# Kernel tuning notes

Measured on AMD Instinct MI355X. Metric: run time of the kernel, lower is better.

Reference implementation:

```python
import jax, jax.numpy as jnp
import numpy as np

NUM_EMBEDDINGS = 1024
EMBEDDING_DIM = 64
COMMIT_COST = 0.25


def setup_inputs() -> dict:
    key = jax.random.key(0)
    k1, k2 = jax.random.split(key)
    latent = jax.random.normal(k1, (32, EMBEDDING_DIM, 32, 32), dtype=jnp.float32)
    embedding_weight = jax.random.normal(k2, (NUM_EMBEDDINGS, EMBEDDING_DIM), dtype=jnp.float32)
    return {"latent": latent, "embedding_weight": embedding_weight}


def reference(latent, embedding_weight):
    # rearrange 'b n j d -> b j d n'; n == embedding_dim
    lat = jnp.transpose(latent, (0, 2, 3, 1))  # [b, j, d, n]
    flat = lat.reshape(-1, EMBEDDING_DIM)      # [T, D]
    # squared-euclidean distances [T, K]
    distances = (
        jnp.sum(flat ** 2, axis=1, keepdims=True)
        + jnp.sum(embedding_weight ** 2, axis=1)
        - 2.0 * flat @ embedding_weight.T
    )
    idx = jnp.argmin(distances, axis=1)                         # [T]
    encodings = jax.nn.one_hot(idx, NUM_EMBEDDINGS, dtype=flat.dtype)  # [T, K]
    quantized_flat = embedding_weight[idx]                      # gather == encodings @ W
    quantized = quantized_flat.reshape(lat.shape)               # [b, j, d, n]

    e_latent_loss = jnp.mean((jax.lax.stop_gradient(quantized) - lat) ** 2)
    loss = COMMIT_COST * e_latent_loss

    # straight-through estimator
    quantized_st = lat + jax.lax.stop_gradient(quantized - lat)

    avg_probs = jnp.mean(encodings, axis=0)
    perplexity = jnp.exp(-jnp.sum(avg_probs * jnp.log(avg_probs + 1e-10)))

    # rearrange back 'b j d n -> b n j d'
    quantized_out = jnp.transpose(quantized_st, (0, 3, 1, 2))
    return quantized_out, loss, perplexity, encodings, distances
```

## Files before the change

### kernel.cpp

```cpp
#include <hip/hip_runtime.h>
#include <cfloat>

#define T_TOTAL 32768
#define DIM 64
#define KCODES 1024

static constexpr long long OFF_Q    = 0;
static constexpr long long OFF_LOSS = 2097152;
static constexpr long long OFF_PERP = 2097153;
static constexpr long long OFF_ENC  = 2097154;
static constexpr long long OFF_DIST = 2097154LL + 33554432LL;


__global__ __launch_bounds__(256) void vq_prep_kernel(const float* __restrict__ W,
                                                      float* __restrict__ ww,
                                                      float* __restrict__ WT) {
    const int tid = threadIdx.x;
    if (blockIdx.x < 256) {
        const int lane = tid & 63;
        const int code = blockIdx.x * 4 + (tid >> 6);
        float v = W[code * DIM + lane];
        float s = v * v;
        #pragma unroll
        for (int off = 32; off > 0; off >>= 1)
            s += __shfl_down(s, off, 64);
        if (lane == 0) ww[code] = s;
    } else {
        const int n = blockIdx.x - 256;
        #pragma unroll
        for (int i = 0; i < 4; ++i) {
            int k = i * 256 + tid;
            WT[n * KCODES + k] = W[k * DIM + n];
        }
    }
}

__global__ __launch_bounds__(256, 4) void vq_main_kernel(const float* __restrict__ lat,
                                                         const float* __restrict__ W,
                                                         const float* __restrict__ ww,
                                                         const float* __restrict__ WT,
                                                         float* __restrict__ out,
                                                         int* __restrict__ counts,
                                                         float* __restrict__ lossSum) {
    __shared__ float xT[64 * 32];
    __shared__ float wS[8 * 512];
    __shared__ float xx[32];
    __shared__ int   selIdx[32];

    const int tid = threadIdx.x;
    const int ct  = tid & 63;
    const int rg  = tid >> 6;
    const int t0  = blockIdx.x * 32;
    const long long base = (long long)(t0 >> 10) * 65536 + (long long)(t0 & 1023);

    #pragma unroll
    for (int i = 0; i < 8; ++i) {
        int e  = i * 256 + tid;
        int n  = e >> 5;
        int tl = e & 31;
        xT[e] = lat[base + (long long)n * 1024 + tl];
    }
    __syncthreads();
    if (tid < 32) {
        float s = 0.f;
        #pragma unroll 8
        for (int n = 0; n < 64; ++n) {
            float v = xT[n * 32 + tid];
            s = fmaf(v, v, s);
        }
        xx[tid] = s;
    }

    float minV[8];
    int   minI[8];
    #pragma unroll
    for (int r = 0; r < 8; ++r) { minV[r] = FLT_MAX; minI[r] = 0; }

    float* __restrict__ distOut = out + OFF_DIST;

    for (int c = 0; c < 2; ++c) {
        float acc[8][8];
        #pragma unroll
        for (int r = 0; r < 8; ++r)
            #pragma unroll
            for (int k = 0; k < 8; ++k) acc[r][k] = 0.f;

        for (int sub = 0; sub < 8; ++sub) {
            __syncthreads();
            #pragma unroll
            for (int i = 0; i < 4; ++i) {
                int e  = i * 256 + tid;
                int n  = e >> 7;
                int k4 = (e & 127) * 4;
                *(float4*)&wS[n * 512 + k4] =
                    *(const float4*)&WT[(sub * 8 + n) * KCODES + c * 512 + k4];
            }
            __syncthreads();

            #pragma unroll
            for (int nn = 0; nn < 8; ++nn) {
                const int ng = sub * 8 + nn;
                float4 a0 = *(const float4*)&xT[ng * 32 + rg * 8];
                float4 a1 = *(const float4*)&xT[ng * 32 + rg * 8 + 4];
                float2 b0 = *(const float2*)&wS[nn * 512 + ct * 2];
                float2 b1 = *(const float2*)&wS[nn * 512 + ct * 2 + 128];
                float2 b2 = *(const float2*)&wS[nn * 512 + ct * 2 + 256];
                float2 b3 = *(const float2*)&wS[nn * 512 + ct * 2 + 384];
                float ar[8] = {a0.x, a0.y, a0.z, a0.w, a1.x, a1.y, a1.z, a1.w};
                float br[8] = {b0.x, b0.y, b1.x, b1.y, b2.x, b2.y, b3.x, b3.y};
                #pragma unroll
                for (int r = 0; r < 8; ++r)
                    #pragma unroll
                    for (int k = 0; k < 8; ++k)
                        acc[r][k] = fmaf(ar[r], br[k], acc[r][k]);
            }
        }

        const int kb = c * 512 + ct * 2;
        float2 wwv[4];
        #pragma unroll
        for (int j = 0; j < 4; ++j)
            wwv[j] = *(const float2*)&ww[kb + j * 128];
        #pragma unroll
        for (int r = 0; r < 8; ++r) {
            const int row = rg * 8 + r;
            const float xxr = xx[row];
            const long long ro = (long long)(t0 + row) * KCODES + kb;
            #pragma unroll
            for (int j = 0; j < 4; ++j) {
                float d0 = (xxr + wwv[j].x) - 2.f * acc[r][2 * j];
                float d1 = (xxr + wwv[j].y) - 2.f * acc[r][2 * j + 1];
                const int ki = kb + j * 128;
                if (d0 < minV[r]) { minV[r] = d0; minI[r] = ki; }
                if (d1 < minV[r]) { minV[r] = d1; minI[r] = ki + 1; }
                *(float2*)&distOut[ro + j * 128] = make_float2(d0, d1);
            }
        }
    }

    #pragma unroll
    for (int r = 0; r < 8; ++r) {
        float v  = minV[r];
        int   i0 = minI[r];
        #pragma unroll
        for (int off = 32; off > 0; off >>= 1) {
            float v2 = __shfl_down(v, off, 64);
            int   i2 = __shfl_down(i0, off, 64);
            if (v2 < v || (v2 == v && i2 < i0)) { v = v2; i0 = i2; }
        }
        if (ct == 0) {
            selIdx[rg * 8 + r] = i0;
            atomicAdd(&counts[i0], 1);
        }
    }
    __syncthreads();

    float* qS = wS;
    #pragma unroll
    for (int i = 0; i < 8; ++i) {
        int e   = i * 256 + tid;
        int row = e >> 6;
        int n   = e & 63;
        qS[row * 65 + n] = W[selIdx[row] * DIM + n];
    }
    __syncthreads();

    float ls = 0.f;
    #pragma unroll
    for (int i = 0; i < 2; ++i) {
        int e2  = i * 256 + tid;
        int n   = e2 >> 3;
        int tl0 = (e2 & 7) * 4;
        float q0 = qS[(tl0 + 0) * 65 + n];
        float q1 = qS[(tl0 + 1) * 65 + n];
        float q2 = qS[(tl0 + 2) * 65 + n];
        float q3 = qS[(tl0 + 3) * 65 + n];
        float x0 = xT[n * 32 + tl0 + 0];
        float x1 = xT[n * 32 + tl0 + 1];
        float x2 = xT[n * 32 + tl0 + 2];
        float x3 = xT[n * 32 + tl0 + 3];
        *(float4*)&out[OFF_Q + base + (long long)n * 1024 + tl0] = make_float4(q0, q1, q2, q3);
        float e0 = q0 - x0; ls = fmaf(e0, e0, ls);
        float e1 = q1 - x1; ls = fmaf(e1, e1, ls);
        float e2d = q2 - x2; ls = fmaf(e2d, e2d, ls);
        float e3 = q3 - x3; ls = fmaf(e3, e3, ls);
    }
    #pragma unroll
    for (int off = 32; off > 0; off >>= 1)
        ls += __shfl_down(ls, off, 64);
    if (ct == 0) atomicAdd(lossSum, ls);

    float* __restrict__ enc = out + OFF_ENC;
    #pragma unroll 4
    for (int i = 0; i < 64; ++i) {
        int e2  = i * 256 + tid;
        int row = e2 >> 9;
        int k2  = (e2 & 511) * 2;
        int sel = selIdx[row];
        float2 v;
        v.x = (k2     == sel) ? 1.f : 0.f;
        v.y = (k2 + 1 == sel) ? 1.f : 0.f;
        *(float2*)&enc[(long long)(t0 + row) * KCODES + k2] = v;
    }
}

__global__ __launch_bounds__(1024) void vq_finalize_kernel(const int* __restrict__ counts,
                                                           const float* __restrict__ lossSum,
                                                           float* __restrict__ out) {
    __shared__ float red[16];
    const int tid = threadIdx.x;
    float p = (float)counts[tid] * (1.0f / 32768.0f);
    float term = p * logf(p + 1e-10f);
    #pragma unroll
    for (int off = 32; off > 0; off >>= 1)
        term += __shfl_down(term, off, 64);
    if ((tid & 63) == 0) red[tid >> 6] = term;
    __syncthreads();
    if (tid == 0) {
        float s = 0.f;
        #pragma unroll
        for (int i = 0; i < 16; ++i) s += red[i];
        out[OFF_PERP] = expf(-s);
        out[OFF_LOSS] = 0.25f * lossSum[0] * (1.0f / 2097152.0f);
    }
}

extern "C" void kernel_launch(void* const* d_in, const int* in_sizes, int n_in,
                              void* d_out, int out_size, void* d_ws, size_t ws_size,
                              hipStream_t stream) {
    (void)in_sizes; (void)n_in; (void)out_size; (void)ws_size;
    const float* lat = (const float*)d_in[0];
    const float* W   = (const float*)d_in[1];
    float* out = (float*)d_out;

    int*   counts  = (int*)d_ws;
    float* ww      = (float*)((char*)d_ws + 4096);
    float* lossSum = (float*)((char*)d_ws + 8192);
    float* WT      = (float*)((char*)d_ws + 12288);

    hipMemsetAsync(d_ws, 0, 8192 + 16, stream);

    vq_prep_kernel<<<320, 256, 0, stream>>>(W, ww, WT);
    vq_main_kernel<<<1024, 256, 0, stream>>>(lat, W, ww, WT, out, counts, lossSum);
    vq_finalize_kernel<<<1, 1024, 0, stream>>>(counts, lossSum, out);
}
```

Before: 398.9 us.

## Read codebook directly from global, nontemporal stores, register-based one-hot writes

The main kernel drops the shared-memory staging of the transposed codebook and its per-subtile barriers. It now reads W^T straight from global/L2 in four 256-code chunks with a smaller 8x4 accumulator tile. The distance and one-hot encoding outputs use nontemporal stores, and each wave writes its own rows using the selected index broadcast in registers. The latent norm is fused into the load through shared atomics. The aim is to cut barriers and register pressure and to stream the large outputs past the cache, at the cost of more global loads per FMA.

```diff
diff --git a/kernel.cpp b/kernel.cpp
--- a/kernel.cpp
+++ b/kernel.cpp
@@ -4,6 +4,8 @@
 #define T_TOTAL 32768
 #define DIM 64
 #define KCODES 1024
+
+typedef float f32x2 __attribute__((ext_vector_type(2)));
 
 static constexpr long long OFF_Q    = 0;
 static constexpr long long OFF_LOSS = 2097152;
@@ -43,9 +45,9 @@
                                                          int* __restrict__ counts,
                                                          float* __restrict__ lossSum) {
     __shared__ float xT[64 * 32];
-    __shared__ float wS[8 * 512];
     __shared__ float xx[32];
-    __shared__ int   selIdx[32];
+    __shared__ float qS[32 * 65];
+    __shared__ int   selS[32];
 
     const int tid = threadIdx.x;
     const int ct  = tid & 63;
@@ -53,23 +55,22 @@
     const int t0  = blockIdx.x * 32;
     const long long base = (long long)(t0 >> 10) * 65536 + (long long)(t0 & 1023);
 
-    #pragma unroll
-    for (int i = 0; i < 8; ++i) {
-        int e  = i * 256 + tid;
-        int n  = e >> 5;
-        int tl = e & 31;
-        xT[e] = lat[base + (long long)n * 1024 + tl];
-    }
-    __syncthreads();
-    if (tid < 32) {
-        float s = 0.f;
-        #pragma unroll 8
-        for (int n = 0; n < 64; ++n) {
-            float v = xT[n * 32 + tid];
-            s = fmaf(v, v, s);
-        }
-        xx[tid] = s;
-    }
+    if (tid < 32) xx[tid] = 0.f;
+    __syncthreads();
+    {
+        float sp = 0.f;
+        #pragma unroll
+        for (int i = 0; i < 8; ++i) {
+            int e  = i * 256 + tid;
+            int n  = e >> 5;
+            int tl = e & 31;
+            float v = lat[base + (long long)n * 1024 + tl];
+            xT[e] = v;
+            sp = fmaf(v, v, sp);
+        }
+        atomicAdd(&xx[tid & 31], sp);
+    }
+    __syncthreads();
 
     float minV[8];
     int   minI[8];
@@ -78,66 +79,53 @@
 
     float* __restrict__ distOut = out + OFF_DIST;
 
-    for (int c = 0; c < 2; ++c) {
-        float acc[8][8];
+    for (int c = 0; c < 4; ++c) {
+        float acc[8][4];
         #pragma unroll
         for (int r = 0; r < 8; ++r)
             #pragma unroll
-            for (int k = 0; k < 8; ++k) acc[r][k] = 0.f;
-
-        for (int sub = 0; sub < 8; ++sub) {
-            __syncthreads();
+            for (int k = 0; k < 4; ++k) acc[r][k] = 0.f;
+
+        const float* __restrict__ wp = WT + c * 256 + ct * 2;
+        #pragma unroll 4
+        for (int n = 0; n < 64; ++n) {
+            float4 a0 = *(const float4*)&xT[n * 32 + rg * 8];
+            float4 a1 = *(const float4*)&xT[n * 32 + rg * 8 + 4];
+            float2 b0 = *(const float2*)&wp[n * KCODES];
+            float2 b1 = *(const float2*)&wp[n * KCODES + 128];
+            float ar[8] = {a0.x, a0.y, a0.z, a0.w, a1.x, a1.y, a1.z, a1.w};
+            float br[4] = {b0.x, b0.y, b1.x, b1.y};
             #pragma unroll
-            for (int i = 0; i < 4; ++i) {
-                int e  = i * 256 + tid;
-                int n  = e >> 7;
-                int k4 = (e & 127) * 4;
-                *(float4*)&wS[n * 512 + k4] =
-                    *(const float4*)&WT[(sub * 8 + n) * KCODES + c * 512 + k4];
-            }
-            __syncthreads();
-
-            #pragma unroll
-            for (int nn = 0; nn < 8; ++nn) {
-                const int ng = sub * 8 + nn;
-                float4 a0 = *(const float4*)&xT[ng * 32 + rg * 8];
-                float4 a1 = *(const float4*)&xT[ng * 32 + rg * 8 + 4];
-                float2 b0 = *(const float2*)&wS[nn * 512 + ct * 2];
-                float2 b1 = *(const float2*)&wS[nn * 512 + ct * 2 + 128];
-                float2 b2 = *(const float2*)&wS[nn * 512 + ct * 2 + 256];
-                float2 b3 = *(const float2*)&wS[nn * 512 + ct * 2 + 384];
-                float ar[8] = {a0.x, a0.y, a0.z, a0.w, a1.x, a1.y, a1.z, a1.w};
-                float br[8] = {b0.x, b0.y, b1.x, b1.y, b2.x, b2.y, b3.x, b3.y};
+            for (int r = 0; r < 8; ++r)
                 #pragma unroll
-                for (int r = 0; r < 8; ++r)
-                    #pragma unroll
-                    for (int k = 0; k < 8; ++k)
-                        acc[r][k] = fmaf(ar[r], br[k], acc[r][k]);
-            }
-        }
-
-        const int kb = c * 512 + ct * 2;
-        float2 wwv[4];
-        #pragma unroll
-        for (int j = 0; j < 4; ++j)
-            wwv[j] = *(const float2*)&ww[kb + j * 128];
+                for (int k = 0; k < 4; ++k)
+                    acc[r][k] = fmaf(ar[r], br[k], acc[r][k]);
+        }
+
+        const int kb = c * 256 + ct * 2;
+        float2 w0 = *(const float2*)&ww[kb];
+        float2 w1 = *(const float2*)&ww[kb + 128];
         #pragma unroll
         for (int r = 0; r < 8; ++r) {
             const int row = rg * 8 + r;
             const float xxr = xx[row];
+            float d0 = (xxr + w0.x) - 2.f * acc[r][0];
+            float d1 = (xxr + w0.y) - 2.f * acc[r][1];
+            float d2 = (xxr + w1.x) - 2.f * acc[r][2];
+            float d3 = (xxr + w1.y) - 2.f * acc[r][3];
+            if (d0 < minV[r]) { minV[r] = d0; minI[r] = kb; }
+            if (d1 < minV[r]) { minV[r] = d1; minI[r] = kb + 1; }
+            if (d2 < minV[r]) { minV[r] = d2; minI[r] = kb + 128; }
+            if (d3 < minV[r]) { minV[r] = d3; minI[r] = kb + 129; }
             const long long ro = (long long)(t0 + row) * KCODES + kb;
-            #pragma unroll
-            for (int j = 0; j < 4; ++j) {
-                float d0 = (xxr + wwv[j].x) - 2.f * acc[r][2 * j];
-                float d1 = (xxr + wwv[j].y) - 2.f * acc[r][2 * j + 1];
-                const int ki = kb + j * 128;
-                if (d0 < minV[r]) { minV[r] = d0; minI[r] = ki; }
-                if (d1 < minV[r]) { minV[r] = d1; minI[r] = ki + 1; }
-                *(float2*)&distOut[ro + j * 128] = make_float2(d0, d1);
-            }
-        }
-    }
-
+            f32x2 v01; v01.x = d0; v01.y = d1;
+            f32x2 v23; v23.x = d2; v23.y = d3;
+            __builtin_nontemporal_store(v01, (f32x2*)&distOut[ro]);
+            __builtin_nontemporal_store(v23, (f32x2*)&distOut[ro + 128]);
+        }
+    }
+
+    int selR[8];
     #pragma unroll
     for (int r = 0; r < 8; ++r) {
         float v  = minV[r];
@@ -148,20 +136,21 @@
             int   i2 = __shfl_down(i0, off, 64);
             if (v2 < v || (v2 == v && i2 < i0)) { v = v2; i0 = i2; }
         }
+        int sel = __shfl(i0, 0, 64);
+        selR[r] = sel;
         if (ct == 0) {
-            selIdx[rg * 8 + r] = i0;
-            atomicAdd(&counts[i0], 1);
-        }
-    }
-    __syncthreads();
-
-    float* qS = wS;
+            selS[rg * 8 + r] = sel;
+            atomicAdd(&counts[sel], 1);
+        }
+    }
+    __syncthreads();
+
     #pragma unroll
     for (int i = 0; i < 8; ++i) {
         int e   = i * 256 + tid;
         int row = e >> 6;
         int n   = e & 63;
-        qS[row * 65 + n] = W[selIdx[row] * DIM + n];
+        qS[row * 65 + n] = W[selS[row] * DIM + n];
     }
     __syncthreads();
 
@@ -175,15 +164,12 @@
         float q1 = qS[(tl0 + 1) * 65 + n];
         float q2 = qS[(tl0 + 2) * 65 + n];
         float q3 = qS[(tl0 + 3) * 65 + n];
-        float x0 = xT[n * 32 + tl0 + 0];
-        float x1 = xT[n * 32 + tl0 + 1];
-        float x2 = xT[n * 32 + tl0 + 2];
-        float x3 = xT[n * 32 + tl0 + 3];
+        float4 xv = *(const float4*)&xT[n * 32 + tl0];
         *(float4*)&out[OFF_Q + base + (long long)n * 1024 + tl0] = make_float4(q0, q1, q2, q3);
-        float e0 = q0 - x0; ls = fmaf(e0, e0, ls);
-        float e1 = q1 - x1; ls = fmaf(e1, e1, ls);
-        float e2d = q2 - x2; ls = fmaf(e2d, e2d, ls);
-        float e3 = q3 - x3; ls = fmaf(e3, e3, ls);
+        float e0 = q0 - xv.x; ls = fmaf(e0, e0, ls);
+        float e1 = q1 - xv.y; ls = fmaf(e1, e1, ls);
+        float e2d = q2 - xv.z; ls = fmaf(e2d, e2d, ls);
+        float e3 = q3 - xv.w; ls = fmaf(e3, e3, ls);
     }
     #pragma unroll
     for (int off = 32; off > 0; off >>= 1)
@@ -191,16 +177,18 @@
     if (ct == 0) atomicAdd(lossSum, ls);
 
     float* __restrict__ enc = out + OFF_ENC;
-    #pragma unroll 4
-    for (int i = 0; i < 64; ++i) {
-        int e2  = i * 256 + tid;
-        int row = e2 >> 9;
-        int k2  = (e2 & 511) * 2;
-        int sel = selIdx[row];
-        float2 v;
-        v.x = (k2     == sel) ? 1.f : 0.f;
-        v.y = (k2 + 1 == sel) ? 1.f : 0.f;
-        *(float2*)&enc[(long long)(t0 + row) * KCODES + k2] = v;
+    #pragma unroll
+    for (int r = 0; r < 8; ++r) {
+        const int sel = selR[r];
+        const long long rowbase = (long long)(t0 + rg * 8 + r) * KCODES;
+        #pragma unroll
+        for (int i = 0; i < 8; ++i) {
+            int k2 = (i * 64 + ct) * 2;
+            f32x2 v;
+            v.x = (k2     == sel) ? 1.f : 0.f;
+            v.y = (k2 + 1 == sel) ? 1.f : 0.f;
+            __builtin_nontemporal_store(v, (f32x2*)&enc[rowbase + k2]);
+        }
     }
 }
 
@@ -238,7 +226,7 @@
     float* lossSum = (float*)((char*)d_ws + 8192);
     float* WT      = (float*)((char*)d_ws + 12288);
 
-    hipMemsetAsync(d_ws, 0, 8192 + 16, stream);
+    (void)hipMemsetAsync(d_ws, 0, 8192 + 16, stream);
 
     vq_prep_kernel<<<320, 256, 0, stream>>>(W, ww, WT);
     vq_main_kernel<<<1024, 256, 0, stream>>>(lat, W, ww, WT, out, counts, lossSum);
```

After: 400.1 us. Within noise of the previous version (+0.3%).
